# Kernel optimization log

Hardware: AMD Instinct MI355X
Metric: run time of the kernel (lower is better)

## Reference

```python
import jax, jax.numpy as jnp
import numpy as np


def setup_inputs() -> dict:
    key = jax.random.key(0)
    ks = jax.random.split(key, 5)
    B, T, S, D = 4, 32, 320, 768
    return {
        "x": jax.random.normal(ks[0], (B, T, S, D), dtype=jnp.float32),
        "qkv_w": jax.random.normal(ks[1], (D, 3 * D), dtype=jnp.float32) * 0.02,
        "qkv_b": jax.random.normal(ks[2], (3 * D,), dtype=jnp.float32) * 0.02,
        "out_w": jax.random.normal(ks[3], (D, D), dtype=jnp.float32) * 0.02,
        "out_b": jax.random.normal(ks[4], (D,), dtype=jnp.float32) * 0.02,
        "n_latents": 64,
        "n_heads": 12,
    }


def reference(x, qkv_w, qkv_b, out_w, out_b, n_latents, n_heads):
    B, T, S, D = x.shape
    H = n_heads
    hd = D // H
    scale = 1.0 / jnp.sqrt(jnp.asarray(hd, dtype=x.dtype))

    # qkv projection: [B,T,S,3D]
    qkv = jnp.einsum('btsd,de->btse', x, qkv_w) + qkv_b
    q, k, v = jnp.split(qkv, 3, axis=-1)
    # [B,T,S,H,hd]
    q = q.reshape(B, T, S, H, hd)
    k = k.reshape(B, T, S, H, hd)
    v = v.reshape(B, T, S, H, hd)

    # block-sparse mask: latent queries (rows < n_latents) cannot attend to
    # patch keys (cols >= n_latents); everything else allowed
    rows = jnp.arange(S) < n_latents          # latent query rows
    cols = jnp.arange(S) >= n_latents         # patch key cols
    allow = ~(rows[:, None] & cols[None, :])  # [S,S] bool

    # attention scores [B,T,H,Sq,Sk]
    scores = jnp.einsum('btqhd,btkhd->bthqk', q, k) * scale
    scores = jnp.where(allow, scores, -jnp.inf)
    attn = jax.nn.softmax(scores, axis=-1)

    y = jnp.einsum('bthqk,btkhd->btqhd', attn, v).reshape(B, T, S, D)
    return jnp.einsum('btsd,de->btse', y, out_w) + out_b
```

## Files before the change

kernel.cpp:

```cpp
#include <hip/hip_runtime.h>

typedef __attribute__((ext_vector_type(8))) short bf16x8;
typedef __attribute__((ext_vector_type(4))) float f32x4;
typedef __attribute__((ext_vector_type(16))) float f32x16;
typedef __attribute__((address_space(1))) void gvoid_t;
typedef __attribute__((address_space(3))) void lvoid_t;

#define DEVI __device__ __forceinline__

DEVI unsigned short f2bf(float f) {
    unsigned int u = __builtin_bit_cast(unsigned int, f);
    u += 0x7fffu + ((u >> 16) & 1u);
    return (unsigned short)(u >> 16);
}

DEVI unsigned cvt_pk_bf16(float a, float b) {
    unsigned r;
    asm("v_cvt_pk_bf16_f32 %0, %1, %2" : "=v"(r) : "v"(a), "v"(b));
    return r;
}

DEVI f32x4 mfma16(bf16x8 a, bf16x8 b, f32x4 c) {
    return __builtin_amdgcn_mfma_f32_16x16x32_bf16(a, b, c, 0, 0, 0);
}

__global__ void k_convert(const float* __restrict__ in, unsigned short* __restrict__ out, int n8) {
    int i = blockIdx.x * 256 + threadIdx.x;
    if (i >= n8) return;
    const float4* p = (const float4*)in + (size_t)i * 2;
    float4 a = p[0], b = p[1];
    uint4 o;
    o.x = f2bf(a.x) | ((unsigned)f2bf(a.y) << 16);
    o.y = f2bf(a.z) | ((unsigned)f2bf(a.w) << 16);
    o.z = f2bf(b.x) | ((unsigned)f2bf(b.y) << 16);
    o.w = f2bf(b.z) | ((unsigned)f2bf(b.w) << 16);
    *((uint4*)out + i) = o;
}

__global__ void k_transpose(const float* __restrict__ w, unsigned short* __restrict__ wt, int K, int N) {
    __shared__ float tile[32][33];
    int n0 = blockIdx.x * 32, k0 = blockIdx.y * 32;
    int tx = threadIdx.x, ty = threadIdx.y;
#pragma unroll
    for (int r = 0; r < 32; r += 8)
        tile[ty + r][tx] = w[(size_t)(k0 + ty + r) * N + n0 + tx];
    __syncthreads();
#pragma unroll
    for (int r = 0; r < 32; r += 8)
        wt[(size_t)(n0 + ty + r) * K + k0 + tx] = f2bf(tile[tx][ty + r]);
}

template <bool OUT_BF16>
__global__ __launch_bounds__(512, 2) void k_gemm256(const unsigned short* __restrict__ A,
                                                    const unsigned short* __restrict__ Bt,
                                                    const float* __restrict__ bias,
                                                    void* __restrict__ out,
                                                    int M, int N, int K) {
    __shared__ unsigned short smem[65536];

    const int tid = threadIdx.x;
    const int nwg = gridDim.x, bid = blockIdx.x;
    const int q8 = nwg >> 3, r8 = nwg & 7;
    const int xcd = bid & 7, lid = bid >> 3;
    const int swz = ((xcd < r8) ? xcd * (q8 + 1) : r8 * (q8 + 1) + (xcd - r8) * q8) + lid;
    const int ntn = N >> 8;
    const int bm = swz / ntn, bn = swz % ntn;

    const int lane = tid & 63, wid = tid >> 6;
    const int wr = wid >> 2, wc = wid & 3;
    const int lr = lane & 15, lg = lane >> 4;
    const int cswz = (lr & 7) << 3;
    const int col0 = (lg * 8) ^ cswz;

    const int NT = K >> 6;

    const int srowl = tid >> 3;
    const int scole = ((tid & 7) ^ (srowl & 7)) << 3;
    const unsigned short* aSrc = A  + (size_t)(bm * 256 + srowl) * K + scole;
    const unsigned short* bSrc = Bt + (size_t)(bn * 256 + srowl) * K + scole;

#define STG(matOff, srcBase, qq, koff, bufw)                                              \
    __builtin_amdgcn_global_load_lds((gvoid_t*)((srcBase) + (size_t)(qq) * 64 * K + (koff)), \
        (lvoid_t*)(smem + (matOff) + (bufw) * 16384 + (qq) * 4096 + tid * 8), 16, 0, 0)

    f32x4 acc[8][4];
#pragma unroll
    for (int i = 0; i < 8; ++i)
#pragma unroll
        for (int j = 0; j < 4; ++j) acc[i][j] = (f32x4){0.f, 0.f, 0.f, 0.f};

    {
        const int k1 = (NT > 1) ? 64 : 0;
        STG(0, aSrc, 0, 0, 0); STG(0, aSrc, 1, 0, 0); STG(0, aSrc, 2, 0, 0); STG(0, aSrc, 3, 0, 0);
        STG(32768, bSrc, 0, 0, 0); STG(32768, bSrc, 1, 0, 0); STG(32768, bSrc, 2, 0, 0); STG(32768, bSrc, 3, 0, 0);
        STG(0, aSrc, 0, k1, 1); STG(0, aSrc, 2, k1, 1);
        asm volatile("s_waitcnt vmcnt(2)" ::: "memory");
        __builtin_amdgcn_s_barrier();
    }

#pragma unroll 1
    for (int t = 0; t < NT; ++t) {
        const int bufR = t & 1, bufW = bufR ^ 1;
        const int ko1 = (t + 1 < NT) ? (t + 1) * 64 : 0;
        const int ko2 = (t + 2 < NT) ? (t + 2) * 64 : 0;
        const unsigned short* abuf = smem + bufR * 16384;
        const unsigned short* bbuf = smem + 32768 + bufR * 16384;
        bf16x8 af[4][2], bfr[2][2];

#pragma unroll
        for (int mf = 0; mf < 4; ++mf)
#pragma unroll
            for (int kk = 0; kk < 2; ++kk)
                af[mf][kk] = *(const bf16x8*)(abuf + (wr * 128 + mf * 16 + lr) * 64 + (col0 ^ (kk * 32)));
#pragma unroll
        for (int j = 0; j < 2; ++j)
#pragma unroll
            for (int kk = 0; kk < 2; ++kk)
                bfr[j][kk] = *(const bf16x8*)(bbuf + (wc * 64 + j * 16 + lr) * 64 + (col0 ^ (kk * 32)));
        STG(32768, bSrc, 0, ko1, bufW); STG(32768, bSrc, 1, ko1, bufW);
        __builtin_amdgcn_s_barrier();
        asm volatile("s_waitcnt lgkmcnt(0)" ::: "memory");
        __builtin_amdgcn_sched_barrier(0);
        __builtin_amdgcn_s_setprio(1);
#pragma unroll
        for (int mf = 0; mf < 4; ++mf)
#pragma unroll
            for (int j = 0; j < 2; ++j)
#pragma unroll
                for (int kk = 0; kk < 2; ++kk)
                    acc[mf][j] = mfma16(af[mf][kk], bfr[j][kk], acc[mf][j]);
        __builtin_amdgcn_s_setprio(0);
        __builtin_amdgcn_s_barrier();

#pragma unroll
        for (int j = 0; j < 2; ++j)
#pragma unroll
            for (int kk = 0; kk < 2; ++kk)
                bfr[j][kk] = *(const bf16x8*)(bbuf + (wc * 64 + (2 + j) * 16 + lr) * 64 + (col0 ^ (kk * 32)));
        STG(32768, bSrc, 2, ko1, bufW); STG(32768, bSrc, 3, ko1, bufW);
        __builtin_amdgcn_s_barrier();
        asm volatile("s_waitcnt lgkmcnt(0)" ::: "memory");
        __builtin_amdgcn_sched_barrier(0);
        __builtin_amdgcn_s_setprio(1);
#pragma unroll
        for (int mf = 0; mf < 4; ++mf)
#pragma unroll
            for (int j = 0; j < 2; ++j)
#pragma unroll
                for (int kk = 0; kk < 2; ++kk)
                    acc[mf][2 + j] = mfma16(af[mf][kk], bfr[j][kk], acc[mf][2 + j]);
        __builtin_amdgcn_s_setprio(0);
        __builtin_amdgcn_s_barrier();

#pragma unroll
        for (int mf = 0; mf < 4; ++mf)
#pragma unroll
            for (int kk = 0; kk < 2; ++kk)
                af[mf][kk] = *(const bf16x8*)(abuf + (wr * 128 + 64 + mf * 16 + lr) * 64 + (col0 ^ (kk * 32)));
        STG(0, aSrc, 1, ko1, bufW); STG(0, aSrc, 3, ko1, bufW);
        __builtin_amdgcn_s_barrier();
        asm volatile("s_waitcnt lgkmcnt(0)" ::: "memory");
        __builtin_amdgcn_sched_barrier(0);
        __builtin_amdgcn_s_setprio(1);
#pragma unroll
        for (int mf = 0; mf < 4; ++mf)
#pragma unroll
            for (int j = 0; j < 2; ++j)
#pragma unroll
                for (int kk = 0; kk < 2; ++kk)
                    acc[4 + mf][2 + j] = mfma16(af[mf][kk], bfr[j][kk], acc[4 + mf][2 + j]);
        __builtin_amdgcn_s_setprio(0);
        __builtin_amdgcn_s_barrier();

#pragma unroll
        for (int j = 0; j < 2; ++j)
#pragma unroll
            for (int kk = 0; kk < 2; ++kk)
                bfr[j][kk] = *(const bf16x8*)(bbuf + (wc * 64 + j * 16 + lr) * 64 + (col0 ^ (kk * 32)));
        STG(0, aSrc, 0, ko2, bufR); STG(0, aSrc, 2, ko2, bufR);
        __builtin_amdgcn_s_barrier();
        asm volatile("s_waitcnt lgkmcnt(0)" ::: "memory");
        __builtin_amdgcn_sched_barrier(0);
        __builtin_amdgcn_s_setprio(1);
#pragma unroll
        for (int mf = 0; mf < 4; ++mf)
#pragma unroll
            for (int j = 0; j < 2; ++j)
#pragma unroll
                for (int kk = 0; kk < 2; ++kk)
                    acc[4 + mf][j] = mfma16(af[mf][kk], bfr[j][kk], acc[4 + mf][j]);
        __builtin_amdgcn_s_setprio(0);
        asm volatile("s_waitcnt vmcnt(2)" ::: "memory");
        __builtin_amdgcn_s_barrier();
    }
#undef STG

#pragma unroll
    for (int mf = 0; mf < 8; ++mf)
#pragma unroll
        for (int nf = 0; nf < 4; ++nf) {
            int col = bn * 256 + wc * 64 + nf * 16 + lr;
            float bv = bias[col];
#pragma unroll
            for (int i = 0; i < 4; ++i) {
                int row = bm * 256 + wr * 128 + mf * 16 + lg * 4 + i;
                float v = acc[mf][nf][i] + bv;
                if (OUT_BF16)
                    ((unsigned short*)out)[(size_t)row * N + col] = f2bf(v);
                else
                    ((float*)out)[(size_t)row * N + col] = v;
            }
        }
}

__global__ __launch_bounds__(640) void k_attn3(const unsigned short* __restrict__ qkv,
                                               unsigned short* __restrict__ y) {
    int bt = blockIdx.x / 12, h = blockIdx.x % 12;
    const unsigned short* Qg = qkv + (size_t)bt * 320 * 2304 + h * 64;
    const unsigned short* Kg = Qg + 768;
    const unsigned short* Vg = Qg + 1536;

    __shared__ unsigned short Vt[10 * 64 * 40];

    int tid = threadIdx.x, w = tid >> 6, l = tid & 63;
    int q = l & 31, hh = l >> 5;
    int q0 = w * 32;
    int ntile = (w < 2) ? 2 : 10;

    {
        int k = tid >> 1;
        int tt = k >> 5, sk = k & 31;
        int d0 = (tid & 1) * 32;
        const unsigned short* src = Vg + (size_t)k * 2304 + d0;
#pragma unroll
        for (int c = 0; c < 4; ++c) {
            union { uint4 u; unsigned short s[8]; } vv;
            vv.u = *(const uint4*)(src + c * 8);
#pragma unroll
            for (int j = 0; j < 8; ++j) {
                int d = d0 + c * 8 + j;
                Vt[(tt * 64 + d) * 40 + (sk ^ (((d >> 3) & 3) << 3))] = vv.s[j];
            }
        }
    }

    bf16x8 qf[4];
#pragma unroll
    for (int c = 0; c < 4; ++c)
        qf[c] = *(const bf16x8*)(Qg + (size_t)(q0 + q) * 2304 + c * 16 + hh * 8);

    f32x16 o0 = (f32x16)0.f, o1 = (f32x16)0.f;
    float m = -3e38f, lsum = 0.f;
    const float SC = 0.125f * 1.44269504089f;

    __syncthreads();

    for (int t = 0; t < ntile; ++t) {
        int s0 = t * 32;
        bf16x8 kf[4];
#pragma unroll
        for (int c = 0; c < 4; ++c)
            kf[c] = *(const bf16x8*)(Kg + (size_t)(s0 + q) * 2304 + c * 16 + hh * 8);

        f32x16 sacc = (f32x16)0.f;
#pragma unroll
        for (int c = 0; c < 4; ++c)
            sacc = __builtin_amdgcn_mfma_f32_32x32x16_bf16(kf[c], qf[c], sacc, 0, 0, 0);

        float p[16];
#pragma unroll
        for (int r = 0; r < 16; ++r) p[r] = sacc[r] * SC;
        float tm = fmaxf(
            fmaxf(fmaxf(fmaxf(p[0], p[1]), fmaxf(p[2], p[3])),
                  fmaxf(fmaxf(p[4], p[5]), fmaxf(p[6], p[7]))),
            fmaxf(fmaxf(fmaxf(p[8], p[9]), fmaxf(p[10], p[11])),
                  fmaxf(fmaxf(p[12], p[13]), fmaxf(p[14], p[15]))));
        tm = fmaxf(tm, __shfl_xor(tm, 32));
        if (!__all(tm <= m + 8.f)) {
            float mn = fmaxf(m, tm);
            float al = __builtin_amdgcn_exp2f(m - mn);
            lsum *= al;
#pragma unroll
            for (int r = 0; r < 16; ++r) { o0[r] *= al; o1[r] *= al; }
            m = mn;
        }
#pragma unroll
        for (int r = 0; r < 16; ++r) p[r] = __builtin_amdgcn_exp2f(p[r] - m);
        float rs =
            ((p[0] + p[1]) + (p[2] + p[3])) + ((p[4] + p[5]) + (p[6] + p[7])) +
            (((p[8] + p[9]) + (p[10] + p[11])) + ((p[12] + p[13]) + (p[14] + p[15])));
        lsum += rs;

        unsigned a0 = cvt_pk_bf16(p[0], p[1]);
        unsigned a1 = cvt_pk_bf16(p[2], p[3]);
        unsigned b0 = cvt_pk_bf16(p[4], p[5]);
        unsigned b1 = cvt_pk_bf16(p[6], p[7]);
        asm("v_permlane32_swap_b32 %0, %1" : "+v"(a0), "+v"(b0));
        asm("v_permlane32_swap_b32 %0, %1" : "+v"(a1), "+v"(b1));
        unsigned c0 = cvt_pk_bf16(p[8], p[9]);
        unsigned c1 = cvt_pk_bf16(p[10], p[11]);
        unsigned d0 = cvt_pk_bf16(p[12], p[13]);
        unsigned d1 = cvt_pk_bf16(p[14], p[15]);
        asm("v_permlane32_swap_b32 %0, %1" : "+v"(c0), "+v"(d0));
        asm("v_permlane32_swap_b32 %0, %1" : "+v"(c1), "+v"(d1));
        union { unsigned u[4]; bf16x8 v; } pf0, pf1;
        pf0.u[0] = a0; pf0.u[1] = a1; pf0.u[2] = b0; pf0.u[3] = b1;
        pf1.u[0] = c0; pf1.u[1] = c1; pf1.u[2] = d0; pf1.u[3] = d1;

        const unsigned short* vt = Vt + t * 2560;
        {
            int d = q;
            int sw = (d >> 3) & 3;
            bf16x8 va0 = *(const bf16x8*)&vt[d * 40 + ((0 + hh) ^ sw) * 8];
            bf16x8 va1 = *(const bf16x8*)&vt[d * 40 + ((2 + hh) ^ sw) * 8];
            o0 = __builtin_amdgcn_mfma_f32_32x32x16_bf16(va0, pf0.v, o0, 0, 0, 0);
            o0 = __builtin_amdgcn_mfma_f32_32x32x16_bf16(va1, pf1.v, o0, 0, 0, 0);
        }
        {
            int d = 32 + q;
            int sw = (d >> 3) & 3;
            bf16x8 va0 = *(const bf16x8*)&vt[d * 40 + ((0 + hh) ^ sw) * 8];
            bf16x8 va1 = *(const bf16x8*)&vt[d * 40 + ((2 + hh) ^ sw) * 8];
            o1 = __builtin_amdgcn_mfma_f32_32x32x16_bf16(va0, pf0.v, o1, 0, 0, 0);
            o1 = __builtin_amdgcn_mfma_f32_32x32x16_bf16(va1, pf1.v, o1, 0, 0, 0);
        }
    }

    lsum += __shfl_xor(lsum, 32);
    float inv = 1.f / lsum;
    unsigned short* yp = y + (size_t)(bt * 320 + q0 + q) * 768 + h * 64;
#pragma unroll
    for (int r = 0; r < 16; r += 2) {
        int dr = (r & 3) + 8 * (r >> 2) + 4 * hh;
        *(unsigned*)(yp + dr) =
            (unsigned)f2bf(o0[r] * inv) | ((unsigned)f2bf(o0[r + 1] * inv) << 16);
        *(unsigned*)(yp + 32 + dr) =
            (unsigned)f2bf(o1[r] * inv) | ((unsigned)f2bf(o1[r + 1] * inv) << 16);
    }
}

extern "C" void kernel_launch(void* const* d_in, const int* in_sizes, int n_in,
                              void* d_out, int out_size, void* d_ws, size_t ws_size,
                              hipStream_t stream) {
    const float* x     = (const float*)d_in[0];
    const float* qkv_w = (const float*)d_in[1];
    const float* qkv_b = (const float*)d_in[2];
    const float* out_w = (const float*)d_in[3];
    const float* out_b = (const float*)d_in[4];

    const int M = 40960;
    unsigned short* xb  = (unsigned short*)d_ws;
    unsigned short* w1t = xb + (size_t)M * 768;
    unsigned short* w2t = w1t + (size_t)2304 * 768;
    unsigned short* qkv = w2t + (size_t)768 * 768;
    unsigned short* yb  = qkv + (size_t)M * 2304;

    k_convert<<<(M * 768 / 8 + 255) / 256, 256, 0, stream>>>(x, xb, M * 768 / 8);
    k_transpose<<<dim3(2304 / 32, 768 / 32), dim3(32, 8), 0, stream>>>(qkv_w, w1t, 768, 2304);
    k_transpose<<<dim3(768 / 32, 768 / 32), dim3(32, 8), 0, stream>>>(out_w, w2t, 768, 768);

    k_gemm256<true><<<(M / 256) * (2304 / 256), 512, 0, stream>>>(xb, w1t, qkv_b, (void*)qkv, M, 2304, 768);
    k_attn3<<<128 * 12, 640, 0, stream>>>(qkv, yb);
    k_gemm256<false><<<(M / 256) * (768 / 256), 512, 0, stream>>>(yb, w2t, out_b, d_out, M, 768, 768);
}
```

Baseline: 381.9 us.

## Keep B fragments in registers, stage GEMM epilogue via LDS, prefetch K tiles

The GEMM main loop now holds two separate B-fragment register sets, so the fourth sub-step reuses the first one instead of reloading it from LDS. That drops one LDS read phase and one barrier per k-step. The epilogue writes accumulators plus bias into a per-wave LDS buffer and then issues coalesced 16-byte global stores instead of scattered scalar stores. The attention kernel double-buffers K fragments in registers so the next tile's global loads overlap the current tile's compute, at the cost of extra VGPRs and a reused LDS region in the epilogue.

```diff
diff --git a/kernel.cpp b/kernel.cpp
--- a/kernel.cpp
+++ b/kernel.cpp
@@ -105,7 +105,7 @@
         const int ko2 = (t + 2 < NT) ? (t + 2) * 64 : 0;
         const unsigned short* abuf = smem + bufR * 16384;
         const unsigned short* bbuf = smem + 32768 + bufR * 16384;
-        bf16x8 af[4][2], bfr[2][2];
+        bf16x8 af[4][2], b01[2][2], b23[2][2];
 
 #pragma unroll
         for (int mf = 0; mf < 4; ++mf)
@@ -116,7 +116,7 @@
         for (int j = 0; j < 2; ++j)
 #pragma unroll
             for (int kk = 0; kk < 2; ++kk)
-                bfr[j][kk] = *(const bf16x8*)(bbuf + (wc * 64 + j * 16 + lr) * 64 + (col0 ^ (kk * 32)));
+                b01[j][kk] = *(const bf16x8*)(bbuf + (wc * 64 + j * 16 + lr) * 64 + (col0 ^ (kk * 32)));
         STG(32768, bSrc, 0, ko1, bufW); STG(32768, bSrc, 1, ko1, bufW);
         __builtin_amdgcn_s_barrier();
         asm volatile("s_waitcnt lgkmcnt(0)" ::: "memory");
@@ -128,7 +128,7 @@
             for (int j = 0; j < 2; ++j)
 #pragma unroll
                 for (int kk = 0; kk < 2; ++kk)
-                    acc[mf][j] = mfma16(af[mf][kk], bfr[j][kk], acc[mf][j]);
+                    acc[mf][j] = mfma16(af[mf][kk], b01[j][kk], acc[mf][j]);
         __builtin_amdgcn_s_setprio(0);
         __builtin_amdgcn_s_barrier();
 
@@ -136,7 +136,7 @@
         for (int j = 0; j < 2; ++j)
 #pragma unroll
             for (int kk = 0; kk < 2; ++kk)
-                bfr[j][kk] = *(const bf16x8*)(bbuf + (wc * 64 + (2 + j) * 16 + lr) * 64 + (col0 ^ (kk * 32)));
+                b23[j][kk] = *(const bf16x8*)(bbuf + (wc * 64 + (2 + j) * 16 + lr) * 64 + (col0 ^ (kk * 32)));
         STG(32768, bSrc, 2, ko1, bufW); STG(32768, bSrc, 3, ko1, bufW);
         __builtin_amdgcn_s_barrier();
         asm volatile("s_waitcnt lgkmcnt(0)" ::: "memory");
@@ -148,7 +148,7 @@
             for (int j = 0; j < 2; ++j)
 #pragma unroll
                 for (int kk = 0; kk < 2; ++kk)
-                    acc[mf][2 + j] = mfma16(af[mf][kk], bfr[j][kk], acc[mf][2 + j]);
+                    acc[mf][2 + j] = mfma16(af[mf][kk], b23[j][kk], acc[mf][2 + j]);
         __builtin_amdgcn_s_setprio(0);
         __builtin_amdgcn_s_barrier();
 
@@ -168,19 +168,11 @@
             for (int j = 0; j < 2; ++j)
 #pragma unroll
                 for (int kk = 0; kk < 2; ++kk)
-                    acc[4 + mf][2 + j] = mfma16(af[mf][kk], bfr[j][kk], acc[4 + mf][2 + j]);
+                    acc[4 + mf][2 + j] = mfma16(af[mf][kk], b23[j][kk], acc[4 + mf][2 + j]);
         __builtin_amdgcn_s_setprio(0);
         __builtin_amdgcn_s_barrier();
 
-#pragma unroll
-        for (int j = 0; j < 2; ++j)
-#pragma unroll
-            for (int kk = 0; kk < 2; ++kk)
-                bfr[j][kk] = *(const bf16x8*)(bbuf + (wc * 64 + j * 16 + lr) * 64 + (col0 ^ (kk * 32)));
         STG(0, aSrc, 0, ko2, bufR); STG(0, aSrc, 2, ko2, bufR);
-        __builtin_amdgcn_s_barrier();
-        asm volatile("s_waitcnt lgkmcnt(0)" ::: "memory");
-        __builtin_amdgcn_sched_barrier(0);
         __builtin_amdgcn_s_setprio(1);
 #pragma unroll
         for (int mf = 0; mf < 4; ++mf)
@@ -188,32 +180,75 @@
             for (int j = 0; j < 2; ++j)
 #pragma unroll
                 for (int kk = 0; kk < 2; ++kk)
-                    acc[4 + mf][j] = mfma16(af[mf][kk], bfr[j][kk], acc[4 + mf][j]);
+                    acc[4 + mf][j] = mfma16(af[mf][kk], b01[j][kk], acc[4 + mf][j]);
         __builtin_amdgcn_s_setprio(0);
         asm volatile("s_waitcnt vmcnt(2)" ::: "memory");
         __builtin_amdgcn_s_barrier();
     }
 #undef STG
 
-#pragma unroll
-    for (int mf = 0; mf < 8; ++mf)
-#pragma unroll
-        for (int nf = 0; nf < 4; ++nf) {
-            int col = bn * 256 + wc * 64 + nf * 16 + lr;
-            float bv = bias[col];
-#pragma unroll
-            for (int i = 0; i < 4; ++i) {
-                int row = bm * 256 + wr * 128 + mf * 16 + lg * 4 + i;
-                float v = acc[mf][nf][i] + bv;
-                if (OUT_BF16)
-                    ((unsigned short*)out)[(size_t)row * N + col] = f2bf(v);
-                else
-                    ((float*)out)[(size_t)row * N + col] = v;
+    asm volatile("s_waitcnt vmcnt(0)" ::: "memory");
+    float bv[4];
+#pragma unroll
+    for (int nf = 0; nf < 4; ++nf)
+        bv[nf] = bias[bn * 256 + wc * 64 + nf * 16 + lr];
+
+    if (OUT_BF16) {
+        unsigned short* ebuf = smem + wid * 8192;
+#pragma unroll
+        for (int h = 0; h < 2; ++h) {
+#pragma unroll
+            for (int mf4 = 0; mf4 < 4; ++mf4) {
+                int mf = h * 4 + mf4;
+#pragma unroll
+                for (int nf = 0; nf < 4; ++nf)
+#pragma unroll
+                    for (int i = 0; i < 4; ++i)
+                        ebuf[(mf4 * 16 + lg * 4 + i) * 72 + nf * 16 + lr] = f2bf(acc[mf][nf][i] + bv[nf]);
             }
-        }
-}
-
-__global__ __launch_bounds__(640) void k_attn3(const unsigned short* __restrict__ qkv,
+            asm volatile("s_waitcnt lgkmcnt(0)" ::: "memory");
+            __builtin_amdgcn_sched_barrier(0);
+#pragma unroll
+            for (int ps = 0; ps < 8; ++ps) {
+                int rl = ps * 8 + (lane >> 3), ck = lane & 7;
+                uint4 vv = *(const uint4*)&ebuf[rl * 72 + ck * 8];
+                int grow = bm * 256 + wr * 128 + h * 64 + rl;
+                int gcol = bn * 256 + wc * 64 + ck * 8;
+                *(uint4*)&((unsigned short*)out)[(size_t)grow * N + gcol] = vv;
+            }
+            asm volatile("s_waitcnt lgkmcnt(0)" ::: "memory");
+            __builtin_amdgcn_sched_barrier(0);
+        }
+    } else {
+        float* ebuf = (float*)smem + wid * 4096;
+#pragma unroll
+        for (int qq = 0; qq < 4; ++qq) {
+#pragma unroll
+            for (int m2 = 0; m2 < 2; ++m2) {
+                int mf = qq * 2 + m2;
+#pragma unroll
+                for (int nf = 0; nf < 4; ++nf)
+#pragma unroll
+                    for (int i = 0; i < 4; ++i)
+                        ebuf[(m2 * 16 + lg * 4 + i) * 68 + nf * 16 + lr] = acc[mf][nf][i] + bv[nf];
+            }
+            asm volatile("s_waitcnt lgkmcnt(0)" ::: "memory");
+            __builtin_amdgcn_sched_barrier(0);
+#pragma unroll
+            for (int ps = 0; ps < 8; ++ps) {
+                int rl = ps * 4 + (lane >> 4), ck = lane & 15;
+                uint4 vv = *(const uint4*)&ebuf[rl * 68 + ck * 4];
+                int grow = bm * 256 + wr * 128 + qq * 32 + rl;
+                int gcol = bn * 256 + wc * 64 + ck * 4;
+                *(uint4*)&((float*)out)[(size_t)grow * N + gcol] = vv;
+            }
+            asm volatile("s_waitcnt lgkmcnt(0)" ::: "memory");
+            __builtin_amdgcn_sched_barrier(0);
+        }
+    }
+}
+
+__global__ __launch_bounds__(640) void k_attn4(const unsigned short* __restrict__ qkv,
                                                unsigned short* __restrict__ y) {
     int bt = blockIdx.x / 12, h = blockIdx.x % 12;
     const unsigned short* Qg = qkv + (size_t)bt * 320 * 2304 + h * 64;
@@ -253,15 +288,17 @@
     float m = -3e38f, lsum = 0.f;
     const float SC = 0.125f * 1.44269504089f;
 
+    bf16x8 kfA[4], kfB[4];
+    auto loadK = [&](bf16x8 (&kf)[4], int tt) {
+#pragma unroll
+        for (int c = 0; c < 4; ++c)
+            kf[c] = *(const bf16x8*)(Kg + (size_t)(tt * 32 + q) * 2304 + c * 16 + hh * 8);
+    };
+    loadK(kfA, 0);
+
     __syncthreads();
 
-    for (int t = 0; t < ntile; ++t) {
-        int s0 = t * 32;
-        bf16x8 kf[4];
-#pragma unroll
-        for (int c = 0; c < 4; ++c)
-            kf[c] = *(const bf16x8*)(Kg + (size_t)(s0 + q) * 2304 + c * 16 + hh * 8);
-
+    auto process = [&](int t, bf16x8 (&kf)[4]) {
         f32x16 sacc = (f32x16)0.f;
 #pragma unroll
         for (int c = 0; c < 4; ++c)
@@ -324,6 +361,13 @@
             o1 = __builtin_amdgcn_mfma_f32_32x32x16_bf16(va0, pf0.v, o1, 0, 0, 0);
             o1 = __builtin_amdgcn_mfma_f32_32x32x16_bf16(va1, pf1.v, o1, 0, 0, 0);
         }
+    };
+
+    for (int t = 0; t < ntile; t += 2) {
+        loadK(kfB, t + 1);
+        process(t, kfA);
+        loadK(kfA, (t + 2 < 10) ? (t + 2) : 8);
+        process(t + 1, kfB);
     }
 
     lsum += __shfl_xor(lsum, 32);
@@ -360,6 +404,6 @@
     k_transpose<<<dim3(768 / 32, 768 / 32), dim3(32, 8), 0, stream>>>(out_w, w2t, 768, 768);
 
     k_gemm256<true><<<(M / 256) * (2304 / 256), 512, 0, stream>>>(xb, w1t, qkv_b, (void*)qkv, M, 2304, 768);
-    k_attn3<<<128 * 12, 640, 0, stream>>>(qkv, yb);
+    k_attn4<<<128 * 12, 640, 0, stream>>>(qkv, yb);
     k_gemm256<false><<<(M / 256) * (768 / 256), 512, 0, stream>>>(yb, w2t, out_b, d_out, M, 768, 768);
 }
```

Measured after the change: 378.6 us. Within noise of the previous version (-0.9%).
